# Kernel optimization log

Hardware: AMD Instinct MI355X
Metric: run time of the kernel (lower is better)

## Reference

```python
import jax, jax.numpy as jnp
import numpy as np

H = W = 2048

def _conv(x, w, ph, pw):
    # PyTorch Conv2d == cross-correlation, same as lax conv (no kernel flip)
    return jax.lax.conv_general_dilated(
        x, w, (1, 1), [(ph, ph), (pw, pw)],
        dimension_numbers=('NCHW', 'OIHW', 'NCHW'))

def _dir_filters():
    f = np.zeros((8, 1, 3, 3), np.float32)
    f[:, 0, 1, 1] = 1.0
    offs = [(1, 2), (2, 2), (2, 1), (2, 0), (1, 0), (0, 0), (0, 1), (0, 2)]
    for k, (r, c) in enumerate(offs):
        f[k, 0, r, c] = -1.0
    return f

def setup_inputs() -> dict:
    key = jax.random.key(0)
    img = jax.random.uniform(key, (1, 3, H, W), jnp.float32)
    threshold = jnp.ones((1,), jnp.float32)
    # unnormalized scipy.signal.gaussian(5, std=1.0)
    g = np.exp(-0.5 * ((np.arange(5) - 2.0) ** 2)).astype(np.float32)
    gauss_h = jnp.asarray(g.reshape(1, 1, 1, 5))
    gauss_v = jnp.asarray(g.reshape(1, 1, 5, 1))
    sob = np.array([[1, 0, -1], [2, 0, -2], [1, 0, -1]], np.float32)
    sobel_h = jnp.asarray(sob.reshape(1, 1, 3, 3))
    sobel_v = jnp.asarray(sob.T.reshape(1, 1, 3, 3))
    dir_w = jnp.asarray(_dir_filters())
    return dict(img=img, threshold=threshold, gauss_h=gauss_h, gauss_v=gauss_v,
                sobel_h=sobel_h, sobel_v=sobel_v, dir_w=dir_w)

def reference(img, threshold, gauss_h, gauss_v, sobel_h, sobel_v, dir_w):
    def blur(c):
        return _conv(_conv(c, gauss_h, 0, 2), gauss_v, 2, 0)
    br = blur(img[:, 0:1]); bg = blur(img[:, 1:2]); bb = blur(img[:, 2:3])
    blurred_img = jnp.concatenate([br, bg, bb], axis=1)  # [1,3,H,W]
    gx_r = _conv(br, sobel_h, 1, 1); gy_r = _conv(br, sobel_v, 1, 1)
    gx_g = _conv(bg, sobel_h, 1, 1); gy_g = _conv(bg, sobel_v, 1, 1)
    gx_b = _conv(bb, sobel_h, 1, 1); gy_b = _conv(bb, sobel_v, 1, 1)
    grad_mag = (jnp.sqrt(gx_r**2 + gy_r**2)
                + jnp.sqrt(gx_g**2 + gy_g**2)
                + jnp.sqrt(gx_b**2 + gy_b**2))  # [1,1,H,W]
    orient = jnp.arctan2(gy_r + gy_g + gy_b, gx_r + gx_g + gx_b) * (180.0 / 3.14159)
    orient = jnp.round((orient + 180.0) / 45.0) * 45.0  # multiples of 45 in [0,360]
    all_f = _conv(grad_mag, dir_w, 1, 1)  # [1,8,H,W]
    idx_pos = ((orient / 45.0) % 8).astype(jnp.int32)[0, 0]       # [H,W]
    idx_neg = ((orient / 45.0 + 4.0) % 8).astype(jnp.int32)[0, 0]  # [H,W]
    af = all_f[0]  # [8,H,W]
    pos = jnp.take_along_axis(af, idx_pos[None], axis=0)[0]
    neg = jnp.take_along_axis(af, idx_neg[None], axis=0)[0]
    is_max = (jnp.minimum(pos, neg) > 0.0)[None, None]  # [1,1,H,W]
    thin_edges = jnp.where(is_max, grad_mag, 0.0)
    thresholded = jnp.where(thin_edges < threshold, 0.0, thin_edges)
    early_threshold = jnp.where(grad_mag < threshold, 0.0, grad_mag)
    return (blurred_img, grad_mag, orient, thin_edges, thresholded, early_threshold)
```

## Files before the change

### kernel.cpp

```cpp
#include <hip/hip_runtime.h>

#define HH 2048
#define WW 2048
#define HWN (HH * WW)

#define T1F 0.41421317376f
#define T2F 2.41420676750f
#define EPSC 2.0e-5f

#define DYPACK 425u
#define DXPACK 36890u

__device__ __forceinline__ void finish_block(
    float thrf,
    float* __restrict__ grad, float* __restrict__ orient,
    float* __restrict__ thin, float* __restrict__ thresh,
    float* __restrict__ early,
    float (*gmb)[66], float (*sxb)[64], float (*syb)[64])
{
#pragma clang fp contract(fast)
    const int tx = threadIdx.x;
    const int ty = threadIdx.y;
    const int x0 = blockIdx.x * 64;
    const int y0 = blockIdx.y * 16;
    const float orient_scale = (float)(180.0 / 3.14159);

    for (int j = 0; j < 4; ++j) {
        const int rr = ty + 4 * j;
        const int y = y0 + rr;
        const int x = x0 + tx;
        const size_t idx = (size_t)y * WW + x;

        const float gm  = gmb[rr + 1][tx + 1];
        const float sxf = sxb[rr][tx];
        const float syf = syb[rr][tx];

        const float axv = fabsf(sxf), ayv = fabsf(syf);
        const float d1 = ayv - T1F * axv;
        const float d2 = ayv - T2F * axv;
        const float eps = EPSC * (axv + ayv);
        int m;
        if (fabsf(d1) > eps && fabsf(d2) > eps) {
            const bool nx = (__float_as_uint(sxf) >> 31) != 0u;
            const bool ny = (__float_as_uint(syf) >> 31) != 0u;
            if (d1 < 0.0f)      m = nx ? (ny ? 0 : 8) : 4;
            else if (d2 > 0.0f) m = ny ? 2 : 6;
            else                m = nx ? (ny ? 1 : 7) : (ny ? 3 : 5);
        } else {
            const float o = atan2f(syf, sxf) * orient_scale;
            m = (int)rintf((o + 180.0f) / 45.0f);
        }
        const int k = m & 7;
        const int dy = (int)((DYPACK >> (2 * k)) & 3u) - 1;
        const int dx = (int)((DXPACK >> (2 * k)) & 3u) - 1;

        const float gnk  = gmb[rr + 1 + dy][tx + 1 + dx];
        const float gnkn = gmb[rr + 1 - dy][tx + 1 - dx];
        const float pos = gm - gnk;
        const float neg = gm - gnkn;
        const float mn = fminf(pos, neg);
        const float del = 4.0e-6f * (4.0f + gm + fmaxf(gnk, gnkn));

        float tv;
        if (mn > del)          tv = gm;
        else if (mn < -del)    tv = 0.0f;
        else if (gm < 14.2f)   tv = gm * 0.5f;
        else                   tv = (mn > 0.0f) ? gm : 0.0f;

        grad[idx]   = gm;
        orient[idx] = 45.0f * (float)m;
        early[idx]  = (gm < thrf) ? 0.0f : gm;
        thin[idx]   = tv;
        thresh[idx] = (tv < thrf) ? 0.0f : tv;
    }
}

__device__ __forceinline__ void do_grad_edge(int r, int c, int ch, int x0, int y0,
    float (*bb)[68], float (*gmb)[66], float (*sxb)[64], float (*syb)[64])
{
#pragma clang fp contract(off)
    float add = 0.0f, gxs = 0.0f, gys = 0.0f;
    const int gy = y0 - 1 + r, gx = x0 - 1 + c;
    const bool inb = (gy >= 0 && gy < HH && gx >= 0 && gx < WW);
    if (inb) {
        const float a00 = bb[r + 0][c + 0];
        const float a01 = bb[r + 0][c + 1];
        const float a02 = bb[r + 0][c + 2];
        const float a10 = bb[r + 1][c + 0];
        const float a12 = bb[r + 1][c + 2];
        const float a20 = bb[r + 2][c + 0];
        const float a21 = bb[r + 2][c + 1];
        const float a22 = bb[r + 2][c + 2];
        gxs = (a00 - a02) + 2.0f * (a10 - a12) + (a20 - a22);
        gys = (a00 - a20) + 2.0f * (a01 - a21) + (a02 - a22);
        add = sqrtf(gxs * gxs + gys * gys);
    }
    if (ch == 0) gmb[r][c] = add;
    else         gmb[r][c] = gmb[r][c] + add;
    if (r >= 1 && r <= 16 && c >= 1 && c <= 64) {
        if (ch == 0) { sxb[r - 1][c - 1] = gxs;                 syb[r - 1][c - 1] = gys; }
        else         { sxb[r - 1][c - 1] = sxb[r - 1][c - 1] + gxs;
                       syb[r - 1][c - 1] = syb[r - 1][c - 1] + gys; }
    }
}

__device__ void canny_body_edge(
    const float* __restrict__ img,
    const float* __restrict__ gh, const float* __restrict__ gv,
    float* __restrict__ blurred,
    float* bufA, float* bufB,
    float (*gmb)[66], float (*sxb)[64], float (*syb)[64])
{
#pragma clang fp contract(off)
    const int tx = threadIdx.x;
    const int ty = threadIdx.y;
    const int tid = ty * 64 + tx;
    const int x0 = blockIdx.x * 64;
    const int y0 = blockIdx.y * 16;

    float (*raw)[72] = reinterpret_cast<float (*)[72]>(bufA);
    float (*bb)[68]  = reinterpret_cast<float (*)[68]>(bufA);
    float (*hb)[68]  = reinterpret_cast<float (*)[68]>(bufB);

    const float g0 = gh[0], g1 = gh[1], g2 = gh[2], g3 = gh[3], g4 = gh[4];
    const float v0 = gv[0], v1 = gv[1], v2 = gv[2], v3 = gv[3], v4 = gv[4];

    for (int ch = 0; ch < 3; ++ch) {
        const float* __restrict__ src = img + (size_t)ch * HWN;

        for (int rr = ty; rr < 24; rr += 4) {
            const int gy = y0 - 4 + rr;
            for (int cc = tx; cc < 72; cc += 64) {
                const int gx = x0 - 4 + cc;
                float v = 0.0f;
                if (gy >= 0 && gy < HH && gx >= 0 && gx < WW)
                    v = src[(size_t)gy * WW + gx];
                raw[rr][cc] = v;
            }
        }
        __syncthreads();

        for (int rr = ty; rr < 24; rr += 4) {
            float acc = g0 * raw[rr][tx + 0];
            acc = acc + g1 * raw[rr][tx + 1];
            acc = acc + g2 * raw[rr][tx + 2];
            acc = acc + g3 * raw[rr][tx + 3];
            acc = acc + g4 * raw[rr][tx + 4];
            hb[rr][tx] = acc;
        }
        if (tid < 96) {
            const int rr = tid >> 2, c = 64 + (tid & 3);
            float acc = g0 * raw[rr][c + 0];
            acc = acc + g1 * raw[rr][c + 1];
            acc = acc + g2 * raw[rr][c + 2];
            acc = acc + g3 * raw[rr][c + 3];
            acc = acc + g4 * raw[rr][c + 4];
            hb[rr][c] = acc;
        }
        __syncthreads();

        for (int r = ty; r < 20; r += 4) {
            const int gy = y0 - 2 + r;
            for (int c = tx; c < 68; c += 64) {
                const int gx = x0 - 2 + c;
                float v = 0.0f;
                if (gy >= 0 && gy < HH && gx >= 0 && gx < WW) {
                    float acc = v0 * hb[r + 0][c];
                    acc = acc + v1 * hb[r + 1][c];
                    acc = acc + v2 * hb[r + 2][c];
                    acc = acc + v3 * hb[r + 3][c];
                    acc = acc + v4 * hb[r + 4][c];
                    v = acc;
                }
                bb[r][c] = v;
            }
        }
        __syncthreads();

        {
            float* __restrict__ dst = blurred + (size_t)ch * HWN;
            for (int j = 0; j < 4; ++j) {
                const int rr = ty + 4 * j;
                dst[(size_t)(y0 + rr) * WW + (x0 + tx)] = bb[rr + 2][tx + 2];
            }
        }

        for (int r = ty; r < 18; r += 4)
            for (int c = tx; c < 66; c += 64)
                do_grad_edge(r, c, ch, x0, y0, bb, gmb, sxb, syb);
        __syncthreads();
    }
}

__device__ void canny_body_int(
    const float* __restrict__ img,
    const float* __restrict__ gh, const float* __restrict__ gv,
    float* __restrict__ blurred,
    float* bufA, float* bufB,
    float (*gmb)[66], float (*sxb)[64], float (*syb)[64])
{
#pragma clang fp contract(fast)
    const int tx = threadIdx.x;
    const int ty = threadIdx.y;
    const int tid = ty * 64 + tx;
    const int x0 = blockIdx.x * 64;
    const int y0 = blockIdx.y * 16;

    const float (*raw)[72] = reinterpret_cast<const float (*)[72]>(bufA);
    float (*bb)[68] = reinterpret_cast<float (*)[68]>(bufB);

    const float g0 = gh[0], g1 = gh[1], g2 = gh[2], g3 = gh[3], g4 = gh[4];
    const float v0 = gv[0], v1 = gv[1], v2 = gv[2], v3 = gv[3], v4 = gv[4];

    float gmr[5] = {0.f, 0.f, 0.f, 0.f, 0.f};
    float sxr[5] = {0.f, 0.f, 0.f, 0.f, 0.f};
    float syr[5] = {0.f, 0.f, 0.f, 0.f, 0.f};
    float gmt = 0.f, sxt = 0.f, syt = 0.f;

    const int r0 = tid / 18, c0 = tid - r0 * 18;
    const int t1 = tid + 256;
    const int r1 = t1 / 18, c1 = t1 - r1 * 18;
    const bool has2 = (t1 < 432);
    const size_t tileoff = (size_t)(y0 - 4) * WW + (x0 - 4);

    {
        const float* srow = img + tileoff;
        __builtin_amdgcn_global_load_lds(
            (const __attribute__((address_space(1))) void*)(srow + (size_t)r0 * WW + c0 * 4),
            (__attribute__((address_space(3))) void*)(bufA + tid * 4), 16, 0, 0);
        if (has2)
            __builtin_amdgcn_global_load_lds(
                (const __attribute__((address_space(1))) void*)(srow + (size_t)r1 * WW + c1 * 4),
                (__attribute__((address_space(3))) void*)(bufA + t1 * 4), 16, 0, 0);
    }
    __syncthreads();

    for (int ch = 0; ch < 3; ++ch) {
        {
            const int rbase = 5 * ty;
            float h[9];
#pragma unroll
            for (int kk = 0; kk < 9; ++kk) {
                const float* rp = &raw[rbase + kk][tx];
                h[kk] = g0 * rp[0] + g1 * rp[1] + g2 * rp[2] + g3 * rp[3] + g4 * rp[4];
            }
#pragma unroll
            for (int kk = 0; kk < 5; ++kk)
                bb[rbase + kk][tx] = v0 * h[kk] + v1 * h[kk + 1] + v2 * h[kk + 2]
                                   + v3 * h[kk + 3] + v4 * h[kk + 4];
        }
        if (tid < 16) {
            const int c  = 64 + (tid & 3);
            const int rb = 5 * (tid >> 2);
            float h[9];
#pragma unroll
            for (int kk = 0; kk < 9; ++kk) {
                const float* rp = &raw[rb + kk][c];
                h[kk] = g0 * rp[0] + g1 * rp[1] + g2 * rp[2] + g3 * rp[3] + g4 * rp[4];
            }
#pragma unroll
            for (int kk = 0; kk < 5; ++kk)
                bb[rb + kk][c] = v0 * h[kk] + v1 * h[kk + 1] + v2 * h[kk + 2]
                              + v3 * h[kk + 3] + v4 * h[kk + 4];
        }
        __syncthreads();

        if (ch < 2) {
            const float* srow = img + (size_t)(ch + 1) * HWN + tileoff;
            __builtin_amdgcn_global_load_lds(
                (const __attribute__((address_space(1))) void*)(srow + (size_t)r0 * WW + c0 * 4),
                (__attribute__((address_space(3))) void*)(bufA + tid * 4), 16, 0, 0);
            if (has2)
                __builtin_amdgcn_global_load_lds(
                    (const __attribute__((address_space(1))) void*)(srow + (size_t)r1 * WW + c1 * 4),
                    (__attribute__((address_space(3))) void*)(bufA + t1 * 4), 16, 0, 0);
        }

        {
            float* __restrict__ dst = blurred + (size_t)ch * HWN;
#pragma unroll
            for (int j = 0; j < 4; ++j) {
                const int rr = ty + 4 * j;
                dst[(size_t)(y0 + rr) * WW + (x0 + tx)] = bb[rr + 2][tx + 2];
            }
        }

#pragma unroll
        for (int i = 0; i < 5; ++i) {
            const int r = ty + 4 * i;
            if (r < 18) {
                const float a00 = bb[r][tx],     a01 = bb[r][tx + 1],     a02 = bb[r][tx + 2];
                const float a10 = bb[r + 1][tx],                          a12 = bb[r + 1][tx + 2];
                const float a20 = bb[r + 2][tx], a21 = bb[r + 2][tx + 1], a22 = bb[r + 2][tx + 2];
                const float gxs = (a00 - a02) + 2.0f * (a10 - a12) + (a20 - a22);
                const float gys = (a00 - a20) + 2.0f * (a01 - a21) + (a02 - a22);
                gmr[i] += sqrtf(gxs * gxs + gys * gys);
                sxr[i] += gxs;
                syr[i] += gys;
            }
        }
        if (tid < 36) {
            const int r = tid >> 1, c = 64 + (tid & 1);
            const float a00 = bb[r][c],     a01 = bb[r][c + 1],     a02 = bb[r][c + 2];
            const float a10 = bb[r + 1][c],                         a12 = bb[r + 1][c + 2];
            const float a20 = bb[r + 2][c], a21 = bb[r + 2][c + 1], a22 = bb[r + 2][c + 2];
            const float gxs = (a00 - a02) + 2.0f * (a10 - a12) + (a20 - a22);
            const float gys = (a00 - a20) + 2.0f * (a01 - a21) + (a02 - a22);
            gmt += sqrtf(gxs * gxs + gys * gys);
            sxt += gxs;
            syt += gys;
        }

        if (ch < 2) __syncthreads();
    }

#pragma unroll
    for (int i = 0; i < 5; ++i) {
        const int r = ty + 4 * i;
        if (r < 18) {
            gmb[r][tx] = gmr[i];
            if (r >= 1 && r <= 16 && tx >= 1) {
                sxb[r - 1][tx - 1] = sxr[i];
                syb[r - 1][tx - 1] = syr[i];
            }
        }
    }
    if (tid < 36) {
        const int r = tid >> 1, c = 64 + (tid & 1);
        gmb[r][c] = gmt;
        if (r >= 1 && r <= 16 && c <= 64) {
            sxb[r - 1][c - 1] = sxt;
            syb[r - 1][c - 1] = syt;
        }
    }
    __syncthreads();
}

__global__ __launch_bounds__(256) void canny_fused(
    const float* __restrict__ img,
    const float* __restrict__ thrp,
    const float* __restrict__ gh,
    const float* __restrict__ gv,
    float* __restrict__ blurred,
    float* __restrict__ grad,
    float* __restrict__ orient,
    float* __restrict__ thin,
    float* __restrict__ thresh,
    float* __restrict__ early)
{
    __shared__ float bufA[24 * 72];
    __shared__ float bufB[24 * 68];
    __shared__ float gmb[18][66];
    __shared__ float sxb[16][64];
    __shared__ float syb[16][64];

    const float thrf = thrp[0];
    const bool edge = (blockIdx.x == 0) | (blockIdx.x == gridDim.x - 1) |
                      (blockIdx.y == 0) | (blockIdx.y == gridDim.y - 1);
    if (edge)
        canny_body_edge(img, gh, gv, blurred, bufA, bufB, gmb, sxb, syb);
    else
        canny_body_int(img, gh, gv, blurred, bufA, bufB, gmb, sxb, syb);

    finish_block(thrf, grad, orient, thin, thresh, early, gmb, sxb, syb);
}

extern "C" void kernel_launch(void* const* d_in, const int* in_sizes, int n_in,
                              void* d_out, int out_size, void* d_ws, size_t ws_size,
                              hipStream_t stream)
{
    const float* img = (const float*)d_in[0];
    const float* thr = (const float*)d_in[1];
    const float* gh  = (const float*)d_in[2];
    const float* gv  = (const float*)d_in[3];

    float* out     = (float*)d_out;
    float* blurred = out;
    float* grad    = out + (size_t)3 * HWN;
    float* orient  = out + (size_t)4 * HWN;
    float* thin    = out + (size_t)5 * HWN;
    float* thresh  = out + (size_t)6 * HWN;
    float* early   = out + (size_t)7 * HWN;

    dim3 blk(64, 4, 1);
    dim3 grd(WW / 64, HH / 16, 1);
    canny_fused<<<grd, blk, 0, stream>>>(img, thr, gh, gv,
                                         blurred, grad, orient, thin, thresh, early);
}
```

Baseline: 254.5 us.

## Load all three channels up front into per-channel LDS buffers, cut barriers

Replaces the per-channel global_load_lds pipeline with register-staged float4 loads of all three channels issued together, then stores them to three separate LDS raw buffers. Blur for all channels runs before a single barrier, and the blurred-store and Sobel phases follow without per-channel syncs. The goal is more memory-level parallelism and fewer __syncthreads. In exchange, LDS use roughly triples (about 36KB per block), which may lower occupancy, and register pressure rises from the staging registers.

```diff
diff --git a/kernel.cpp b/kernel.cpp
--- a/kernel.cpp
+++ b/kernel.cpp
@@ -10,6 +10,9 @@
 
 #define DYPACK 425u
 #define DXPACK 36890u
+
+#define RAWF 1728
+#define BBF  1360
 
 __device__ __forceinline__ void finish_block(
     float thrf,
@@ -196,7 +199,7 @@
     const float* __restrict__ img,
     const float* __restrict__ gh, const float* __restrict__ gv,
     float* __restrict__ blurred,
-    float* bufA, float* bufB,
+    float* rawBase, float* bbBase,
     float (*gmb)[66], float (*sxb)[64], float (*syb)[64])
 {
 #pragma clang fp contract(fast)
@@ -206,36 +209,39 @@
     const int x0 = blockIdx.x * 64;
     const int y0 = blockIdx.y * 16;
 
-    const float (*raw)[72] = reinterpret_cast<const float (*)[72]>(bufA);
-    float (*bb)[68] = reinterpret_cast<float (*)[68]>(bufB);
-
     const float g0 = gh[0], g1 = gh[1], g2 = gh[2], g3 = gh[3], g4 = gh[4];
     const float v0 = gv[0], v1 = gv[1], v2 = gv[2], v3 = gv[3], v4 = gv[4];
-
-    float gmr[5] = {0.f, 0.f, 0.f, 0.f, 0.f};
-    float sxr[5] = {0.f, 0.f, 0.f, 0.f, 0.f};
-    float syr[5] = {0.f, 0.f, 0.f, 0.f, 0.f};
-    float gmt = 0.f, sxt = 0.f, syt = 0.f;
 
     const int r0 = tid / 18, c0 = tid - r0 * 18;
     const int t1 = tid + 256;
     const int r1 = t1 / 18, c1 = t1 - r1 * 18;
     const bool has2 = (t1 < 432);
     const size_t tileoff = (size_t)(y0 - 4) * WW + (x0 - 4);
-
-    {
-        const float* srow = img + tileoff;
-        __builtin_amdgcn_global_load_lds(
-            (const __attribute__((address_space(1))) void*)(srow + (size_t)r0 * WW + c0 * 4),
-            (__attribute__((address_space(3))) void*)(bufA + tid * 4), 16, 0, 0);
+    const size_t off0 = (size_t)r0 * WW + (size_t)(c0 * 4);
+    const size_t off1 = (size_t)r1 * WW + (size_t)(c1 * 4);
+
+    float4 stg[3][2];
+#pragma unroll
+    for (int ch = 0; ch < 3; ++ch) {
+        const float* s = img + (size_t)ch * HWN + tileoff;
+        stg[ch][0] = *reinterpret_cast<const float4*>(s + off0);
         if (has2)
-            __builtin_amdgcn_global_load_lds(
-                (const __attribute__((address_space(1))) void*)(srow + (size_t)r1 * WW + c1 * 4),
-                (__attribute__((address_space(3))) void*)(bufA + t1 * 4), 16, 0, 0);
+            stg[ch][1] = *reinterpret_cast<const float4*>(s + off1);
+    }
+#pragma unroll
+    for (int ch = 0; ch < 3; ++ch) {
+        float* d = rawBase + ch * RAWF;
+        *reinterpret_cast<float4*>(d + tid * 4) = stg[ch][0];
+        if (has2)
+            *reinterpret_cast<float4*>(d + t1 * 4) = stg[ch][1];
     }
     __syncthreads();
 
-    for (int ch = 0; ch < 3; ++ch) {
+#pragma unroll
+    for (int ch = 0; ch < 3; ++ch) {
+        const float (*raw)[72] =
+            reinterpret_cast<const float (*)[72]>(rawBase + ch * RAWF);
+        float (*bb)[68] = reinterpret_cast<float (*)[68]>(bbBase + ch * BBF);
         {
             const int rbase = 5 * ty;
             float h[9];
@@ -263,26 +269,24 @@
                 bb[rb + kk][c] = v0 * h[kk] + v1 * h[kk + 1] + v2 * h[kk + 2]
                               + v3 * h[kk + 3] + v4 * h[kk + 4];
         }
-        __syncthreads();
-
-        if (ch < 2) {
-            const float* srow = img + (size_t)(ch + 1) * HWN + tileoff;
-            __builtin_amdgcn_global_load_lds(
-                (const __attribute__((address_space(1))) void*)(srow + (size_t)r0 * WW + c0 * 4),
-                (__attribute__((address_space(3))) void*)(bufA + tid * 4), 16, 0, 0);
-            if (has2)
-                __builtin_amdgcn_global_load_lds(
-                    (const __attribute__((address_space(1))) void*)(srow + (size_t)r1 * WW + c1 * 4),
-                    (__attribute__((address_space(3))) void*)(bufA + t1 * 4), 16, 0, 0);
-        }
-
-        {
-            float* __restrict__ dst = blurred + (size_t)ch * HWN;
-#pragma unroll
-            for (int j = 0; j < 4; ++j) {
-                const int rr = ty + 4 * j;
-                dst[(size_t)(y0 + rr) * WW + (x0 + tx)] = bb[rr + 2][tx + 2];
-            }
+    }
+    __syncthreads();
+
+    float gmr[5] = {0.f, 0.f, 0.f, 0.f, 0.f};
+    float sxr[5] = {0.f, 0.f, 0.f, 0.f, 0.f};
+    float syr[5] = {0.f, 0.f, 0.f, 0.f, 0.f};
+    float gmt = 0.f, sxt = 0.f, syt = 0.f;
+
+#pragma unroll
+    for (int ch = 0; ch < 3; ++ch) {
+        const float (*bb)[68] =
+            reinterpret_cast<const float (*)[68]>(bbBase + ch * BBF);
+
+        float* __restrict__ dst = blurred + (size_t)ch * HWN;
+#pragma unroll
+        for (int j = 0; j < 4; ++j) {
+            const int rr = ty + 4 * j;
+            dst[(size_t)(y0 + rr) * WW + (x0 + tx)] = bb[rr + 2][tx + 2];
         }
 
 #pragma unroll
@@ -310,8 +314,6 @@
             sxt += gxs;
             syt += gys;
         }
-
-        if (ch < 2) __syncthreads();
     }
 
 #pragma unroll
@@ -348,8 +350,8 @@
     float* __restrict__ thresh,
     float* __restrict__ early)
 {
-    __shared__ float bufA[24 * 72];
-    __shared__ float bufB[24 * 68];
+    __shared__ float raw3[3 * RAWF];
+    __shared__ float bb3[3 * BBF];
     __shared__ float gmb[18][66];
     __shared__ float sxb[16][64];
     __shared__ float syb[16][64];
@@ -358,9 +360,9 @@
     const bool edge = (blockIdx.x == 0) | (blockIdx.x == gridDim.x - 1) |
                       (blockIdx.y == 0) | (blockIdx.y == gridDim.y - 1);
     if (edge)
-        canny_body_edge(img, gh, gv, blurred, bufA, bufB, gmb, sxb, syb);
+        canny_body_edge(img, gh, gv, blurred, raw3, bb3, gmb, sxb, syb);
     else
-        canny_body_int(img, gh, gv, blurred, bufA, bufB, gmb, sxb, syb);
+        canny_body_int(img, gh, gv, blurred, raw3, bb3, gmb, sxb, syb);
 
     finish_block(thrf, grad, orient, thin, thresh, early, gmb, sxb, syb);
 }
```

Result: slower. 338.4 us (+33.0%).
